# Kernel optimization log

Measured on AMD Instinct MI355X. Metric: run time of the kernel, lower is better.

## Reference

```python
import jax, jax.numpy as jnp
import numpy as np

N_POINTS = 131072   # dense point cloud, batch['points'][0]
N_NODES = 2048      # coarse node set, batch['points'][-1]
NEIGHBOR_SEL = 32   # config['neighbor_sel']


def setup_inputs() -> dict:
    key = jax.random.key(0)
    k1, k2 = jax.random.split(key)
    point_cloud = jax.random.normal(k1, (N_POINTS, 3), dtype=jnp.float32)
    nodes = jax.random.normal(k2, (N_NODES, 3), dtype=jnp.float32)
    return {"point_cloud": point_cloud, "nodes": nodes, "neighbor_sel": NEIGHBOR_SEL}


def _knn1(points, nodes):
    # pairwise squared distances [N, M] = |p|^2 - 2 p.n + |n|^2
    d2 = (jnp.sum(points * points, axis=-1, keepdims=True)
          - 2.0 * (points @ nodes.T)
          + jnp.sum(nodes * nodes, axis=-1)[None, :])
    pcd_id = jnp.argmin(d2, axis=1)          # [N] nearest node per point (k=1 knn)
    min_d2 = jnp.min(d2, axis=1)             # [N] nearest squared distance
    return min_d2, pcd_id


def _grouping(pcd_id, n_nodes, k):
    # Replicates grouping_wrapper: for each node, collect the first k point
    # indices (in point order) assigned to it; unfilled slots stay -1.
    n = pcd_id.shape[0]
    order = jnp.argsort(pcd_id, stable=True)          # stable -> preserves point order within a node
    sorted_ids = pcd_id[order]                        # [N] non-decreasing node ids
    starts = jnp.searchsorted(sorted_ids, jnp.arange(n_nodes))  # group start offsets [M]
    rank = jnp.arange(n) - starts[sorted_ids]         # within-group rank of each point
    col = jnp.where(rank < k, rank, k)                # overflow slots routed to scratch column k
    patch = jnp.full((n_nodes, k + 1), -1, dtype=jnp.int32)
    patch = patch.at[sorted_ids, col].set(order.astype(jnp.int32))
    patch = patch[:, :k]                              # drop scratch column
    return jnp.maximum(patch, 0)                      # patch[patch < 0] = 0


def reference(point_cloud, nodes, neighbor_sel):
    min_d2, pcd_id = _knn1(point_cloud, nodes)
    patch = _grouping(pcd_id, nodes.shape[0], neighbor_sel)
    # pcd_id returned as [1, N, 1] matching knn(pc[None], nodes[None], k=1)
    return min_d2, pcd_id[None, :, None], patch[None]
```

## Files before the change

kernel.cpp:

```cpp
#include <hip/hip_runtime.h>
#include <hip/hip_bf16.h>

#define NPTS   131072
#define NNODES 2048
#define KSEL   32

#define TKNN   256
#define PPT    2
#define PPG_K  (TKNN * PPT)
#define NGRP_K (NPTS / PPG_K)
#define NCHUNK 8
#define CHN    (NNODES / NCHUNK)
#define HALF   (CHN / 2)

#define GSZ    512
#define NG     (NPTS / GSZ)

typedef unsigned int uint;
typedef unsigned short u16;
typedef unsigned long long u64;
typedef float f2 __attribute__((ext_vector_type(2)));

__device__ __forceinline__ f2 splat(float s) { return (f2){s, s}; }

__device__ __forceinline__ uint f2ord(float d) {
    uint b = __float_as_uint(d);
    return (b & 0x80000000u) ? ~b : (b | 0x80000000u);
}
__device__ __forceinline__ float ord2f(uint t) {
    uint b = (t & 0x80000000u) ? (t ^ 0x80000000u) : ~t;
    return __uint_as_float(b);
}

__global__ __launch_bounds__(256) void prep_init(const float* __restrict__ nodes,
                                                 float4* __restrict__ n4,
                                                 u64* __restrict__ knnres) {
    int i = blockIdx.x * 256 + threadIdx.x;
    knnres[i] = ~0ull;
    if (i < NNODES) {
        float x = nodes[3 * i], y = nodes[3 * i + 1], z = nodes[3 * i + 2];
        float nn = __fadd_rn(__fadd_rn(__fmul_rn(x, x), __fmul_rn(y, y)), __fmul_rn(z, z));
        n4[i] = make_float4(x, y, z, nn);
    }
}

__global__ __launch_bounds__(256) void knn_part(const float* __restrict__ pts,
                                                const float4* __restrict__ n4,
                                                u64* __restrict__ knnres) {
    int bid = blockIdx.x;
    int c   = bid & (NCHUNK - 1);
    int g   = bid >> 3;
    int t   = threadIdx.x;

    f2 pp2, nx2, ny2, nz2;
    #pragma unroll
    for (int h = 0; h < 2; ++h) {
        int pid = g * PPG_K + h * TKNN + t;
        float p0 = pts[3 * pid], p1 = pts[3 * pid + 1], p2 = pts[3 * pid + 2];
        float pp = __fadd_rn(__fadd_rn(__fmul_rn(p0, p0), __fmul_rn(p1, p1)),
                             __fmul_rn(p2, p2));
        pp2[h] = pp;
        nx2[h] = __fmul_rn(-2.0f, p0);
        ny2[h] = __fmul_rn(-2.0f, p1);
        nz2[h] = __fmul_rn(-2.0f, p2);
    }

    const float4* np = n4 + c * CHN;
    float bestA[PPT], bestB[PPT];
    int   qbA[PPT],   qbB[PPT];
    #pragma unroll
    for (int p = 0; p < PPT; ++p) {
        bestA[p] = 3.4e38f; bestB[p] = 3.4e38f; qbA[p] = 0; qbB[p] = 0;
    }

    #pragma unroll 2
    for (int jj = 0; jj < HALF; jj += 4) {
        float4 a0 = np[jj + 0];
        float4 a1 = np[jj + 1];
        float4 a2 = np[jj + 2];
        float4 a3 = np[jj + 3];
        float4 b0 = np[HALF + jj + 0];
        float4 b1 = np[HALF + jj + 1];
        float4 b2 = np[HALF + jj + 2];
        float4 b3 = np[HALF + jj + 3];

        f2 dA0, dA1, dA2, dA3, dB0, dB1, dB2, dB3;
        {   f2 m = nx2 * splat(a0.x);
            f2 r = __builtin_elementwise_fma(ny2, splat(a0.y), m);
            r    = __builtin_elementwise_fma(nz2, splat(a0.z), r);
            dA0  = (pp2 + r) + splat(a0.w); }
        {   f2 m = nx2 * splat(a1.x);
            f2 r = __builtin_elementwise_fma(ny2, splat(a1.y), m);
            r    = __builtin_elementwise_fma(nz2, splat(a1.z), r);
            dA1  = (pp2 + r) + splat(a1.w); }
        {   f2 m = nx2 * splat(a2.x);
            f2 r = __builtin_elementwise_fma(ny2, splat(a2.y), m);
            r    = __builtin_elementwise_fma(nz2, splat(a2.z), r);
            dA2  = (pp2 + r) + splat(a2.w); }
        {   f2 m = nx2 * splat(a3.x);
            f2 r = __builtin_elementwise_fma(ny2, splat(a3.y), m);
            r    = __builtin_elementwise_fma(nz2, splat(a3.z), r);
            dA3  = (pp2 + r) + splat(a3.w); }
        {   f2 m = nx2 * splat(b0.x);
            f2 r = __builtin_elementwise_fma(ny2, splat(b0.y), m);
            r    = __builtin_elementwise_fma(nz2, splat(b0.z), r);
            dB0  = (pp2 + r) + splat(b0.w); }
        {   f2 m = nx2 * splat(b1.x);
            f2 r = __builtin_elementwise_fma(ny2, splat(b1.y), m);
            r    = __builtin_elementwise_fma(nz2, splat(b1.z), r);
            dB1  = (pp2 + r) + splat(b1.w); }
        {   f2 m = nx2 * splat(b2.x);
            f2 r = __builtin_elementwise_fma(ny2, splat(b2.y), m);
            r    = __builtin_elementwise_fma(nz2, splat(b2.z), r);
            dB2  = (pp2 + r) + splat(b2.w); }
        {   f2 m = nx2 * splat(b3.x);
            f2 r = __builtin_elementwise_fma(ny2, splat(b3.y), m);
            r    = __builtin_elementwise_fma(nz2, splat(b3.z), r);
            dB3  = (pp2 + r) + splat(b3.w); }

        #pragma unroll
        for (int p = 0; p < PPT; ++p) {
            float eA0 = p ? dA0.y : dA0.x;
            float eA1 = p ? dA1.y : dA1.x;
            float eA2 = p ? dA2.y : dA2.x;
            float eA3 = p ? dA3.y : dA3.x;
            float mA  = fminf(fminf(bestA[p], eA0), eA1);
            float nA  = fminf(fminf(mA, eA2), eA3);
            qbA[p]    = (nA < bestA[p]) ? jj : qbA[p];
            bestA[p]  = nA;

            float eB0 = p ? dB0.y : dB0.x;
            float eB1 = p ? dB1.y : dB1.x;
            float eB2 = p ? dB2.y : dB2.x;
            float eB3 = p ? dB3.y : dB3.x;
            float mB  = fminf(fminf(bestB[p], eB0), eB1);
            float nB  = fminf(fminf(mB, eB2), eB3);
            qbB[p]    = (nB < bestB[p]) ? jj : qbB[p];
            bestB[p]  = nB;
        }
    }

    #pragma unroll
    for (int p = 0; p < PPT; ++p) {
        float bA = bestA[p], bB = bestB[p];
        float b  = fminf(bA, bB);
        int base = (bB < bA) ? (HALF + qbB[p]) : qbA[p];

        float nx = nx2[p], ny = ny2[p], nz = nz2[p], pp = pp2[p];
        float dd[4];
        #pragma unroll
        for (int o = 0; o < 4; ++o) {
            float4 v = np[base + o];
            float m = __fmul_rn(nx, v.x);
            float r = __builtin_fmaf(ny, v.y, m);
            r       = __builtin_fmaf(nz, v.z, r);
            dd[o]   = __fadd_rn(__fadd_rn(pp, r), v.w);
        }
        int off = 3;
        if (dd[2] == b) off = 2;
        if (dd[1] == b) off = 1;
        if (dd[0] == b) off = 0;

        int pid = g * PPG_K + p * TKNN + t;
        u64 key = ((u64)f2ord(b) << 32) | (uint)(c * CHN + base + off);
        atomicMin(&knnres[pid], key);
    }
}

__global__ __launch_bounds__(256) void merge_hist(const u64* __restrict__ knnres,
                                                  float* __restrict__ out_d2,
                                                  float* __restrict__ out_id,
                                                  int* __restrict__ pcd,
                                                  u16* __restrict__ hist16,
                                                  float* __restrict__ patch) {
    __shared__ uint lh[NNODES];
    int g = blockIdx.x, t = threadIdx.x;
    patch[(size_t)g * 256 + t] = 0.0f;
    for (int i = t; i < NNODES; i += 256) lh[i] = 0;
    __syncthreads();

    #pragma unroll
    for (int q = 0; q < GSZ / 256; ++q) {
        int pid = g * GSZ + q * 256 + t;
        u64 key = knnres[pid];
        uint bi = (uint)key;
        float d = ord2f((uint)(key >> 32));
        atomicAdd(&lh[bi], 1u);
        out_d2[pid] = d;
        out_id[pid] = (float)bi;
        pcd[pid]    = (int)bi;
    }
    __syncthreads();
    for (int i = t; i < NNODES; i += 256)
        hist16[(size_t)g * NNODES + i] = (u16)lh[i];
}

__global__ __launch_bounds__(256) void scan_offs(const u16* __restrict__ hist16,
                                                 uint* __restrict__ offs) {
    int t = threadIdx.x, lane = t & 63, wv = t >> 6;
    int node = blockIdx.x * 4 + wv;

    uint v0 = hist16[(size_t)(4 * lane + 0) * NNODES + node];
    uint v1 = hist16[(size_t)(4 * lane + 1) * NNODES + node];
    uint v2 = hist16[(size_t)(4 * lane + 2) * NNODES + node];
    uint v3 = hist16[(size_t)(4 * lane + 3) * NNODES + node];
    uint s = v0 + v1 + v2 + v3;
    uint a = s;
    #pragma unroll
    for (int d = 1; d < 64; d <<= 1) {
        uint y = __shfl_up(a, d, 64);
        if (lane >= d) a += y;
    }
    uint base = a - s;
    uint4 o = make_uint4(base, base + v0, base + v0 + v1, base + v0 + v1 + v2);
    *(uint4*)(offs + (size_t)node * NG + 4 * lane) = o;
}

__global__ __launch_bounds__(256) void scatter_patch(const int* __restrict__ pcd,
                                                     const uint* __restrict__ offs,
                                                     float* __restrict__ patch) {
    __shared__ int ids[GSZ];
    int g = blockIdx.x, t = threadIdx.x;
    ids[t]       = pcd[g * GSZ + t];
    ids[256 + t] = pcd[g * GSZ + 256 + t];
    __syncthreads();

    int i0 = t, i1 = 256 + t;
    int my0 = ids[i0], my1 = ids[i1];
    int r0 = 0, r1 = 0;
    #pragma unroll 8
    for (int j = 0; j < GSZ; ++j) {
        int id = ids[j];
        r0 += (j < i0 && id == my0) ? 1 : 0;
        r1 += (j < i1 && id == my1) ? 1 : 0;
    }
    uint rk0 = offs[(size_t)my0 * NG + g] + (uint)r0;
    uint rk1 = offs[(size_t)my1 * NG + g] + (uint)r1;
    if (rk0 < KSEL) patch[(size_t)my0 * KSEL + rk0] = (float)(g * GSZ + i0);
    if (rk1 < KSEL) patch[(size_t)my1 * KSEL + rk1] = (float)(g * GSZ + i1);
}

extern "C" void kernel_launch(void* const* d_in, const int* in_sizes, int n_in,
                              void* d_out, int out_size, void* d_ws, size_t ws_size,
                              hipStream_t stream) {
    const float* pts   = (const float*)d_in[0];
    const float* nodes = (const float*)d_in[1];

    float* out       = (float*)d_out;
    float* out_d2    = out;
    float* out_id    = out + NPTS;
    float* out_patch = out + 2 * NPTS;

    char* ws = (char*)d_ws;
    u64*   knnres = (u64*) ws;
    u16*   hist16 = (u16*) (ws + (1 << 20));
    uint*  offs   = (uint*) (ws + (2 << 20));
    int*   pcd    = (int*)  (ws + (4 << 20));
    float4* n4    = (float4*)(ws + (4 << 20) + (512 << 10));

    prep_init<<<NPTS / 256, 256, 0, stream>>>(nodes, n4, knnres);
    knn_part<<<NGRP_K * NCHUNK, TKNN, 0, stream>>>(pts, n4, knnres);
    merge_hist<<<NG, 256, 0, stream>>>(knnres, out_d2, out_id, pcd, hist16, out_patch);
    scan_offs<<<NNODES / 4, 256, 0, stream>>>(hist16, offs);
    scatter_patch<<<NG, 256, 0, stream>>>(pcd, offs, out_patch);
}
```

Before: 119.5 us.

## Stage node chunk in LDS, drop prep kernel, replace atomicMin with per-chunk partials

```diff
diff --git a/kernel.cpp b/kernel.cpp
--- a/kernel.cpp
+++ b/kernel.cpp
@@ -32,25 +32,22 @@
     return __uint_as_float(b);
 }
 
-__global__ __launch_bounds__(256) void prep_init(const float* __restrict__ nodes,
-                                                 float4* __restrict__ n4,
-                                                 u64* __restrict__ knnres) {
-    int i = blockIdx.x * 256 + threadIdx.x;
-    knnres[i] = ~0ull;
-    if (i < NNODES) {
-        float x = nodes[3 * i], y = nodes[3 * i + 1], z = nodes[3 * i + 2];
-        float nn = __fadd_rn(__fadd_rn(__fmul_rn(x, x), __fmul_rn(y, y)), __fmul_rn(z, z));
-        n4[i] = make_float4(x, y, z, nn);
-    }
-}
-
-__global__ __launch_bounds__(256) void knn_part(const float* __restrict__ pts,
-                                                const float4* __restrict__ n4,
-                                                u64* __restrict__ knnres) {
+__global__ __launch_bounds__(256, 8) void knn_part(const float* __restrict__ pts,
+                                                   const float* __restrict__ nodes,
+                                                   u64* __restrict__ part) {
+    __shared__ float4 sn4[CHN];
     int bid = blockIdx.x;
     int c   = bid & (NCHUNK - 1);
     int g   = bid >> 3;
     int t   = threadIdx.x;
+
+    {
+        int n = c * CHN + t;
+        float x = nodes[3 * n], y = nodes[3 * n + 1], z = nodes[3 * n + 2];
+        float nn = __fadd_rn(__fadd_rn(__fmul_rn(x, x), __fmul_rn(y, y)),
+                             __fmul_rn(z, z));
+        sn4[t] = make_float4(x, y, z, nn);
+    }
 
     f2 pp2, nx2, ny2, nz2;
     #pragma unroll
@@ -64,8 +61,8 @@
         ny2[h] = __fmul_rn(-2.0f, p1);
         nz2[h] = __fmul_rn(-2.0f, p2);
     }
-
-    const float4* np = n4 + c * CHN;
+    __syncthreads();
+
     float bestA[PPT], bestB[PPT];
     int   qbA[PPT],   qbB[PPT];
     #pragma unroll
@@ -75,14 +72,14 @@
 
     #pragma unroll 2
     for (int jj = 0; jj < HALF; jj += 4) {
-        float4 a0 = np[jj + 0];
-        float4 a1 = np[jj + 1];
-        float4 a2 = np[jj + 2];
-        float4 a3 = np[jj + 3];
-        float4 b0 = np[HALF + jj + 0];
-        float4 b1 = np[HALF + jj + 1];
-        float4 b2 = np[HALF + jj + 2];
-        float4 b3 = np[HALF + jj + 3];
+        float4 a0 = sn4[jj + 0];
+        float4 a1 = sn4[jj + 1];
+        float4 a2 = sn4[jj + 2];
+        float4 a3 = sn4[jj + 3];
+        float4 b0 = sn4[HALF + jj + 0];
+        float4 b1 = sn4[HALF + jj + 1];
+        float4 b2 = sn4[HALF + jj + 2];
+        float4 b3 = sn4[HALF + jj + 3];
 
         f2 dA0, dA1, dA2, dA3, dB0, dB1, dB2, dB3;
         {   f2 m = nx2 * splat(a0.x);
@@ -150,7 +147,7 @@
         float dd[4];
         #pragma unroll
         for (int o = 0; o < 4; ++o) {
-            float4 v = np[base + o];
+            float4 v = sn4[base + o];
             float m = __fmul_rn(nx, v.x);
             float r = __builtin_fmaf(ny, v.y, m);
             r       = __builtin_fmaf(nz, v.z, r);
@@ -163,11 +160,11 @@
 
         int pid = g * PPG_K + p * TKNN + t;
         u64 key = ((u64)f2ord(b) << 32) | (uint)(c * CHN + base + off);
-        atomicMin(&knnres[pid], key);
-    }
-}
-
-__global__ __launch_bounds__(256) void merge_hist(const u64* __restrict__ knnres,
+        part[(size_t)c * NPTS + pid] = key;
+    }
+}
+
+__global__ __launch_bounds__(256) void merge_hist(const u64* __restrict__ part,
                                                   float* __restrict__ out_d2,
                                                   float* __restrict__ out_id,
                                                   int* __restrict__ pcd,
@@ -182,7 +179,12 @@
     #pragma unroll
     for (int q = 0; q < GSZ / 256; ++q) {
         int pid = g * GSZ + q * 256 + t;
-        u64 key = knnres[pid];
+        u64 key = part[pid];
+        #pragma unroll
+        for (int cc = 1; cc < NCHUNK; ++cc) {
+            u64 k2 = part[(size_t)cc * NPTS + pid];
+            key = (k2 < key) ? k2 : key;
+        }
         uint bi = (uint)key;
         float d = ord2f((uint)(key >> 32));
         atomicAdd(&lh[bi], 1u);
@@ -252,15 +254,13 @@
     float* out_patch = out + 2 * NPTS;
 
     char* ws = (char*)d_ws;
-    u64*   knnres = (u64*) ws;
-    u16*   hist16 = (u16*) (ws + (1 << 20));
-    uint*  offs   = (uint*) (ws + (2 << 20));
-    int*   pcd    = (int*)  (ws + (4 << 20));
-    float4* n4    = (float4*)(ws + (4 << 20) + (512 << 10));
-
-    prep_init<<<NPTS / 256, 256, 0, stream>>>(nodes, n4, knnres);
-    knn_part<<<NGRP_K * NCHUNK, TKNN, 0, stream>>>(pts, n4, knnres);
-    merge_hist<<<NG, 256, 0, stream>>>(knnres, out_d2, out_id, pcd, hist16, out_patch);
+    u64*   part   = (u64*) ws;
+    u16*   hist16 = (u16*) (ws + (8 << 20));
+    uint*  offs   = (uint*) (ws + (9 << 20));
+    int*   pcd    = (int*)  (ws + (11 << 20));
+
+    knn_part<<<NGRP_K * NCHUNK, TKNN, 0, stream>>>(pts, nodes, part);
+    merge_hist<<<NG, 256, 0, stream>>>(part, out_d2, out_id, pcd, hist16, out_patch);
     scan_offs<<<NNODES / 4, 256, 0, stream>>>(hist16, offs);
     scatter_patch<<<NG, 256, 0, stream>>>(pcd, offs, out_patch);
 }
```

After: 121.0 us. About the same (+1.3%).
